# Performance work log

Measured on AMD Instinct MI355X. Metric: run time of the kernel, lower is better.

## Reference

```python
import jax, jax.numpy as jnp
import numpy as np

T = 512          # sentence length
D_IN = 449       # 300 (google w2v) + 100 (trained w2v) + 49 (len(cposTable))
H = 512          # lstm hidden_dim
H2 = 256         # hidden_dim2 (mlp head/modifier dim)


def _run_lstm(x, Wih, Whh, b):
    # single-direction LSTM, torch gate order (i, f, g, o); bias = b_ih + b_hh folded.
    hdim = Whh.shape[-1]
    def step(carry, xt):
        h, c = carry
        z = Wih @ xt + Whh @ h + b              # [4H]
        i, f, g, o = jnp.split(z, 4)
        c = jax.nn.sigmoid(f) * c + jax.nn.sigmoid(i) * jnp.tanh(g)
        h = jax.nn.sigmoid(o) * jnp.tanh(c)
        return (h, c), h
    h0 = jnp.zeros((hdim,), x.dtype)
    _, hs = jax.lax.scan(step, (h0, h0), x)
    return hs                                    # [T, H]


def _bilstm_layer(x, Wih, Whh, b):
    # Wih: [2, 4H, Din]; dir 0 forward, dir 1 backward
    fwd = _run_lstm(x, Wih[0], Whh[0], b[0])
    bwd = _run_lstm(x[::-1], Wih[1], Whh[1], b[1])[::-1]
    return jnp.concatenate([fwd, bwd], axis=-1)  # [T, 2H]


def setup_inputs() -> dict:
    key = jax.random.key(0)
    ks = jax.random.split(key, 20)
    s = 0.1  # keep LSTM gates out of deep saturation
    inp = {
        "x": jax.random.normal(ks[0], (T, D_IN), jnp.float32),
        "e1l0_Wih": s * jax.random.normal(ks[1], (2, 4 * H, D_IN), jnp.float32),
        "e1l0_Whh": s * jax.random.normal(ks[2], (2, 4 * H, H), jnp.float32),
        "e1l0_b":   s * jax.random.normal(ks[3], (2, 4 * H), jnp.float32),
        "e1l1_Wih": s * jax.random.normal(ks[4], (2, 4 * H, 2 * H), jnp.float32),
        "e1l1_Whh": s * jax.random.normal(ks[5], (2, 4 * H, H), jnp.float32),
        "e1l1_b":   s * jax.random.normal(ks[6], (2, 4 * H), jnp.float32),
        "e2l0_Wih": s * jax.random.normal(ks[7], (2, 4 * H, 2 * H), jnp.float32),
        "e2l0_Whh": s * jax.random.normal(ks[8], (2, 4 * H, H), jnp.float32),
        "e2l0_b":   s * jax.random.normal(ks[9], (2, 4 * H), jnp.float32),
        "e2l1_Wih": s * jax.random.normal(ks[10], (2, 4 * H, 2 * H), jnp.float32),
        "e2l1_Whh": s * jax.random.normal(ks[11], (2, 4 * H, H), jnp.float32),
        "e2l1_b":   s * jax.random.normal(ks[12], (2, 4 * H), jnp.float32),
        "Wh": s * jax.random.normal(ks[13], (H2, 2 * H), jnp.float32),
        "bh": s * jax.random.normal(ks[14], (H2,), jnp.float32),
        "Wm": s * jax.random.normal(ks[15], (H2, 2 * H), jnp.float32),
        "bm": s * jax.random.normal(ks[16], (H2,), jnp.float32),
        "w_score": s * jax.random.normal(ks[17], (H2,), jnp.float32),
        "b_score": s * jax.random.normal(ks[18], (1,), jnp.float32),
    }
    return inp


def reference(x, e1l0_Wih, e1l0_Whh, e1l0_b, e1l1_Wih, e1l1_Whh, e1l1_b,
              e2l0_Wih, e2l0_Whh, e2l0_b, e2l1_Wih, e2l1_Whh, e2l1_b,
              Wh, bh, Wm, bm, w_score, b_score):
    # encoder 1 (2-layer bi-LSTM); dropout is inference-mode identity
    h = _bilstm_layer(x, e1l0_Wih, e1l0_Whh, e1l0_b)
    h = _bilstm_layer(h, e1l1_Wih, e1l1_Whh, e1l1_b)
    # encoder 2 (2-layer bi-LSTM)
    h = _bilstm_layer(h, e2l0_Wih, e2l0_Whh, e2l0_b)
    h = _bilstm_layer(h, e2l1_Wih, e2l1_Whh, e2l1_b)
    # prepend zero ROOT row -> [T+1, 2H]
    h = jnp.concatenate([jnp.zeros((1, h.shape[1]), h.dtype), h], axis=0)
    # vectorized all-pairs edge scorer: tanh(heads[i] + mods[j]) @ w + b
    heads = h @ Wh.T + bh                         # [N, H2]
    mods = h @ Wm.T + bm                          # [N, H2]
    pair = jnp.tanh(heads[:, None, :] + mods[None, :, :])   # [N, N, H2]
    score = jnp.einsum('ijh,h->ij', pair, w_score) + b_score[0]
    n = score.shape[0]
    eye = jnp.eye(n, dtype=bool)
    score = jnp.where(eye, jnp.zeros((), score.dtype), score)  # diag = 0
    return score                                   # [T+1, T+1]
```

## Files before the change

kernel.cpp:

```cpp
#include <hip/hip_runtime.h>
#include <math.h>

#define TLEN 512
#define G4   2048
#define HID  512
#define D2H  1024
#define MLP  256
#define NR   513
#define NWG  32

typedef unsigned long long ull;

__device__ __forceinline__ float sigm(float x) { return 1.0f / (1.0f + __expf(-x)); }
__device__ __forceinline__ float tanh_(float x) { return 1.0f - 2.0f / (1.0f + __expf(2.0f * x)); }

__global__ __launch_bounds__(256) void pad_rows(const float* __restrict__ src,
                                                float* __restrict__ dst,
                                                int rows, int ksrc, int kdst) {
    int idx = blockIdx.x * 256 + threadIdx.x;
    if (idx >= rows * kdst) return;
    int r = idx / kdst, k = idx - r * kdst;
    dst[idx] = (k < ksrc) ? src[(long)r * ksrc + k] : 0.0f;
}

__global__ __launch_bounds__(256) void gemm_btn(
    const float* __restrict__ X, int ldx,
    const float* __restrict__ W, int ldw, long wsd,
    const float* __restrict__ bias, int bsd,
    float* __restrict__ Out, long osd,
    int M, int N, int K)
{
    int dir = blockIdx.z;
    const float* Wd = W + (long)dir * wsd;
    const float* bd = bias + (long)dir * bsd;
    float* Od = Out + (long)dir * osd;
    int n0 = blockIdx.x * 64, m0 = blockIdx.y * 64;
    __shared__ float As[16][68], Bs[16][68];
    int tid = threadIdx.x;
    int ti = tid >> 4, tj = tid & 15;
    int lr = tid >> 2, lq = tid & 3;
    float acc[4][4] = {};
    for (int k0 = 0; k0 < K; k0 += 16) {
        int mrow = m0 + lr;
        float4 xa = make_float4(0.f, 0.f, 0.f, 0.f);
        if (mrow < M) xa = *(const float4*)(X + (long)mrow * ldx + k0 + lq * 4);
        As[lq * 4 + 0][lr] = xa.x; As[lq * 4 + 1][lr] = xa.y;
        As[lq * 4 + 2][lr] = xa.z; As[lq * 4 + 3][lr] = xa.w;
        float4 wa = *(const float4*)(Wd + (long)(n0 + lr) * ldw + k0 + lq * 4);
        Bs[lq * 4 + 0][lr] = wa.x; Bs[lq * 4 + 1][lr] = wa.y;
        Bs[lq * 4 + 2][lr] = wa.z; Bs[lq * 4 + 3][lr] = wa.w;
        __syncthreads();
#pragma unroll
        for (int kk = 0; kk < 16; ++kk) {
            float4 a = *(const float4*)&As[kk][ti * 4];
            float4 b = *(const float4*)&Bs[kk][tj * 4];
            acc[0][0] += a.x * b.x; acc[0][1] += a.x * b.y; acc[0][2] += a.x * b.z; acc[0][3] += a.x * b.w;
            acc[1][0] += a.y * b.x; acc[1][1] += a.y * b.y; acc[1][2] += a.y * b.z; acc[1][3] += a.y * b.w;
            acc[2][0] += a.z * b.x; acc[2][1] += a.z * b.y; acc[2][2] += a.z * b.z; acc[2][3] += a.z * b.w;
            acc[3][0] += a.w * b.x; acc[3][1] += a.w * b.y; acc[3][2] += a.w * b.z; acc[3][3] += a.w * b.w;
        }
        __syncthreads();
    }
#pragma unroll
    for (int i = 0; i < 4; ++i) {
        int m = m0 + ti * 4 + i;
        if (m < M) {
#pragma unroll
            for (int j = 0; j < 4; ++j) {
                int n = n0 + tj * 4 + j;
                Od[(long)m * N + n] = acc[i][j] + bd[n];
            }
        }
    }
}

__global__ __launch_bounds__(256, 1) void lstm_rec(
    const float* __restrict__ Whh,
    const float* __restrict__ Zpre,
    ull* __restrict__ Ytag,
    float* __restrict__ Hout,
    unsigned tagbase)
{
    int wg = blockIdx.x;
    int dir = blockIdx.y;
    int tid = threadIdx.x;
    int rl = tid >> 2;
    int kp = tid & 3;
    int g = rl >> 4;
    int jj = rl & 15;
    int row_global = g * 512 + wg * 16 + jj;

    const float* wrow = Whh + ((long)dir * G4 + row_global) * HID + kp * 128;
    float4 w4[32];
#pragma unroll
    for (int u = 0; u < 32; ++u) w4[u] = *(const float4*)(wrow + u * 4);

    __shared__ float hs[528];
    __shared__ float zs[64];
    float c_reg = 0.0f;

    for (int s = 0; s < TLEN; ++s) {
        int t_x = dir ? (TLEN - 1 - s) : s;
        float z_i = 0.f, z_f = 0.f, z_g = 0.f, z_o = 0.f;
        if (tid < 16) {
            const float* zp = Zpre + ((long)dir * TLEN + t_x) * G4 + wg * 16 + tid;
            z_i = zp[0]; z_f = zp[512]; z_g = zp[1024]; z_o = zp[1536];
        }
        if (s > 0) {
            int rrow = dir ? (TLEN - s) : (s - 1);
            const ull* src = Ytag + (long)rrow * D2H + dir * HID;
            unsigned expect = tagbase + (unsigned)rrow;
            int e = tid * 2;
            ull v0 = __hip_atomic_load(src + e, __ATOMIC_RELAXED, __HIP_MEMORY_SCOPE_AGENT);
            while ((unsigned)(v0 >> 32) != expect) {
                __builtin_amdgcn_s_sleep(1);
                v0 = __hip_atomic_load(src + e, __ATOMIC_RELAXED, __HIP_MEMORY_SCOPE_AGENT);
            }
            ull v1 = __hip_atomic_load(src + e + 1, __ATOMIC_RELAXED, __HIP_MEMORY_SCOPE_AGENT);
            while ((unsigned)(v1 >> 32) != expect) {
                __builtin_amdgcn_s_sleep(1);
                v1 = __hip_atomic_load(src + e + 1, __ATOMIC_RELAXED, __HIP_MEMORY_SCOPE_AGENT);
            }
            int base = e + (e >> 7) * 4;
            hs[base]     = __uint_as_float((unsigned)v0);
            hs[base + 1] = __uint_as_float((unsigned)v1);
            __syncthreads();
            const float* hp = &hs[kp * 132];
            float z = 0.0f;
#pragma unroll
            for (int u = 0; u < 32; ++u) {
                float4 hv = *(const float4*)(hp + u * 4);
                z = fmaf(w4[u].x, hv.x, z); z = fmaf(w4[u].y, hv.y, z);
                z = fmaf(w4[u].z, hv.z, z); z = fmaf(w4[u].w, hv.w, z);
            }
            z += __shfl_xor(z, 1);
            z += __shfl_xor(z, 2);
            if (kp == 0) zs[rl] = z;
            __syncthreads();
        } else {
            if (tid < 64) zs[tid] = 0.0f;
            __syncthreads();
        }
        if (tid < 16) {
            float zi = zs[tid]      + z_i;
            float zf = zs[16 + tid] + z_f;
            float zg = zs[32 + tid] + z_g;
            float zo = zs[48 + tid] + z_o;
            float ig = sigm(zi), fg = sigm(zf), gv = tanh_(zg), og = sigm(zo);
            c_reg = fg * c_reg + ig * gv;
            float h = og * tanh_(c_reg);
            int j = wg * 16 + tid;
            ull pk = ((ull)(tagbase + (unsigned)t_x) << 32) | (ull)__float_as_uint(h);
            __hip_atomic_store(Ytag + (long)t_x * D2H + dir * HID + j, pk,
                               __ATOMIC_RELAXED, __HIP_MEMORY_SCOPE_AGENT);
            Hout[(long)t_x * D2H + dir * HID + j] = h;
        }
    }
}

__global__ __launch_bounds__(256) void pair_score(
    const float* __restrict__ heads, const float* __restrict__ mods,
    const float* __restrict__ w_s, const float* __restrict__ b_s,
    float* __restrict__ out)
{
    __shared__ float hsh[16][260], msh[16][260], wsh[256];
    int tid = threadIdx.x;
    int i0 = blockIdx.y * 16, j0 = blockIdx.x * 16;
    int r = tid >> 4, cq = tid & 15;
#pragma unroll
    for (int u = 0; u < 4; ++u) {
        int col = cq * 16 + u * 4;
        if (col < MLP) {
            float4 hv = make_float4(0.f, 0.f, 0.f, 0.f), mv = hv;
            if (i0 + r < NR) hv = *(const float4*)(heads + (long)(i0 + r) * MLP + col);
            if (j0 + r < NR) mv = *(const float4*)(mods + (long)(j0 + r) * MLP + col);
            *(float4*)&hsh[r][col] = hv;
            *(float4*)&msh[r][col] = mv;
        }
    }
    wsh[tid] = w_s[tid];
    __syncthreads();
    int ti = tid >> 4, tj = tid & 15;
    float acc = 0.0f;
#pragma unroll 4
    for (int h = 0; h < MLP; ++h) {
        acc += wsh[h] * tanh_(hsh[ti][h] + msh[tj][h]);
    }
    int i = i0 + ti, j = j0 + tj;
    if (i < NR && j < NR) out[(long)i * NR + j] = (i == j) ? 0.0f : (acc + b_s[0]);
}

extern "C" void kernel_launch(void* const* d_in, const int* in_sizes, int n_in,
                              void* d_out, int out_size, void* d_ws, size_t ws_size,
                              hipStream_t stream)
{
    const float* x = (const float*)d_in[0];
    float* ws = (float*)d_ws;
    float* Xpad  = ws;
    float* Wpad  = Xpad + 512 * 512;
    float* Z     = Wpad + 2 * 2048 * 512;
    ull*   YtagA = (ull*)(Z + 2 * 512 * 2048);
    ull*   YtagB = YtagA + 512 * 1024;
    float* bufAc = (float*)(YtagB + 512 * 1024);
    float* bufBc = bufAc + 512 * 1024;
    float* Hcat  = bufBc + 512 * 1024;
    float* heads = Hcat + 513 * 1024;
    float* mods  = heads + 513 * 256;

    hipMemsetAsync(YtagA, 0, 2 * 512 * 1024 * sizeof(ull), stream);
    hipMemsetAsync(Hcat, 0, D2H * sizeof(float), stream);

    pad_rows<<<dim3(1024), 256, 0, stream>>>(x, Xpad, 512, 449, 512);
    pad_rows<<<dim3(8192), 256, 0, stream>>>((const float*)d_in[1], Wpad, 2 * 2048, 449, 512);

    dim3 gz(G4 / 64, TLEN / 64, 2);
    dim3 gr(NWG, 2);

    gemm_btn<<<gz, 256, 0, stream>>>(Xpad, 512, Wpad, 512, (long)G4 * 512,
                                     (const float*)d_in[3], G4, Z, (long)TLEN * G4, TLEN, G4, 512);
    lstm_rec<<<gr, 256, 0, stream>>>((const float*)d_in[2], Z, YtagA, bufAc, 1u * 4096u);

    gemm_btn<<<gz, 256, 0, stream>>>(bufAc, D2H, (const float*)d_in[4], D2H, (long)G4 * D2H,
                                     (const float*)d_in[6], G4, Z, (long)TLEN * G4, TLEN, G4, D2H);
    lstm_rec<<<gr, 256, 0, stream>>>((const float*)d_in[5], Z, YtagB, bufBc, 2u * 4096u);

    gemm_btn<<<gz, 256, 0, stream>>>(bufBc, D2H, (const float*)d_in[7], D2H, (long)G4 * D2H,
                                     (const float*)d_in[9], G4, Z, (long)TLEN * G4, TLEN, G4, D2H);
    lstm_rec<<<gr, 256, 0, stream>>>((const float*)d_in[8], Z, YtagA, bufAc, 3u * 4096u);

    gemm_btn<<<gz, 256, 0, stream>>>(bufAc, D2H, (const float*)d_in[10], D2H, (long)G4 * D2H,
                                     (const float*)d_in[12], G4, Z, (long)TLEN * G4, TLEN, G4, D2H);
    lstm_rec<<<gr, 256, 0, stream>>>((const float*)d_in[11], Z, YtagB, Hcat + D2H, 4u * 4096u);

    gemm_btn<<<dim3(MLP / 64, 9, 1), 256, 0, stream>>>(Hcat, D2H, (const float*)d_in[13], D2H, 0,
                                                       (const float*)d_in[14], 0, heads, 0, NR, MLP, D2H);
    gemm_btn<<<dim3(MLP / 64, 9, 1), 256, 0, stream>>>(Hcat, D2H, (const float*)d_in[15], D2H, 0,
                                                       (const float*)d_in[16], 0, mods, 0, NR, MLP, D2H);

    pair_score<<<dim3(33, 33), 256, 0, stream>>>(heads, mods, (const float*)d_in[17],
                                                 (const float*)d_in[18], (float*)d_out);
}
```

Before: 4.477 ms.

## Spread LSTM recurrence over 128 workgroups per direction, reading Whh from cache

The recurrent kernel now uses 128 workgroups per direction instead of 32, each owning 4 hidden units (16 gate rows). Each gate row is split across 16 threads that reduce with shuffles. The Whh weights are no longer held in registers and are reloaded from global memory (L2/cache) every step. The intent is to shorten per-step latency and use more CUs, at the cost of more cross-workgroup polling on the tagged h vector and repeated weight reads each step. It assumes all 256 workgroups stay co-resident.

```diff
diff --git a/kernel.cpp b/kernel.cpp
--- a/kernel.cpp
+++ b/kernel.cpp
@@ -7,7 +7,7 @@
 #define D2H  1024
 #define MLP  256
 #define NR   513
-#define NWG  32
+#define NWG  128
 
 typedef unsigned long long ull;
 
@@ -84,26 +84,22 @@
     int wg = blockIdx.x;
     int dir = blockIdx.y;
     int tid = threadIdx.x;
-    int rl = tid >> 2;
-    int kp = tid & 3;
-    int g = rl >> 4;
-    int jj = rl & 15;
-    int row_global = g * 512 + wg * 16 + jj;
-
-    const float* wrow = Whh + ((long)dir * G4 + row_global) * HID + kp * 128;
-    float4 w4[32];
-#pragma unroll
-    for (int u = 0; u < 32; ++u) w4[u] = *(const float4*)(wrow + u * 4);
-
-    __shared__ float hs[528];
-    __shared__ float zs[64];
+    int c = tid & 15;
+    int r = tid >> 4;
+    int g = r >> 2, i = r & 3;
+    int rowg = g * 512 + wg * 4 + i;
+
+    const float* pw = Whh + ((long)dir * G4 + rowg) * HID + c * 32;
+
+    __shared__ float hs[576];
+    __shared__ float zs[16];
     float c_reg = 0.0f;
 
     for (int s = 0; s < TLEN; ++s) {
         int t_x = dir ? (TLEN - 1 - s) : s;
         float z_i = 0.f, z_f = 0.f, z_g = 0.f, z_o = 0.f;
-        if (tid < 16) {
-            const float* zp = Zpre + ((long)dir * TLEN + t_x) * G4 + wg * 16 + tid;
+        if (tid < 4) {
+            const float* zp = Zpre + ((long)dir * TLEN + t_x) * G4 + wg * 4 + tid;
             z_i = zp[0]; z_f = zp[512]; z_g = zp[1024]; z_o = zp[1536];
         }
         if (s > 0) {
@@ -111,45 +107,51 @@
             const ull* src = Ytag + (long)rrow * D2H + dir * HID;
             unsigned expect = tagbase + (unsigned)rrow;
             int e = tid * 2;
-            ull v0 = __hip_atomic_load(src + e, __ATOMIC_RELAXED, __HIP_MEMORY_SCOPE_AGENT);
+            ull v0 = __hip_atomic_load(src + e,     __ATOMIC_RELAXED, __HIP_MEMORY_SCOPE_AGENT);
+            ull v1 = __hip_atomic_load(src + e + 1, __ATOMIC_RELAXED, __HIP_MEMORY_SCOPE_AGENT);
             while ((unsigned)(v0 >> 32) != expect) {
                 __builtin_amdgcn_s_sleep(1);
                 v0 = __hip_atomic_load(src + e, __ATOMIC_RELAXED, __HIP_MEMORY_SCOPE_AGENT);
             }
-            ull v1 = __hip_atomic_load(src + e + 1, __ATOMIC_RELAXED, __HIP_MEMORY_SCOPE_AGENT);
             while ((unsigned)(v1 >> 32) != expect) {
                 __builtin_amdgcn_s_sleep(1);
                 v1 = __hip_atomic_load(src + e + 1, __ATOMIC_RELAXED, __HIP_MEMORY_SCOPE_AGENT);
             }
-            int base = e + (e >> 7) * 4;
+            int base = e + ((e >> 5) << 2);
             hs[base]     = __uint_as_float((unsigned)v0);
             hs[base + 1] = __uint_as_float((unsigned)v1);
             __syncthreads();
-            const float* hp = &hs[kp * 132];
-            float z = 0.0f;
-#pragma unroll
-            for (int u = 0; u < 32; ++u) {
-                float4 hv = *(const float4*)(hp + u * 4);
-                z = fmaf(w4[u].x, hv.x, z); z = fmaf(w4[u].y, hv.y, z);
-                z = fmaf(w4[u].z, hv.z, z); z = fmaf(w4[u].w, hv.w, z);
-            }
-            z += __shfl_xor(z, 1);
-            z += __shfl_xor(z, 2);
-            if (kp == 0) zs[rl] = z;
+            const float* hp = &hs[c * 36];
+            float a0 = 0.f, a1 = 0.f;
+#pragma unroll
+            for (int u = 0; u < 8; u += 2) {
+                float4 w0 = *(const float4*)(pw + u * 4);
+                float4 h0 = *(const float4*)(hp + u * 4);
+                float4 w1 = *(const float4*)(pw + u * 4 + 4);
+                float4 h1 = *(const float4*)(hp + u * 4 + 4);
+                a0 = fmaf(w0.x, h0.x, a0); a0 = fmaf(w0.y, h0.y, a0);
+                a0 = fmaf(w0.z, h0.z, a0); a0 = fmaf(w0.w, h0.w, a0);
+                a1 = fmaf(w1.x, h1.x, a1); a1 = fmaf(w1.y, h1.y, a1);
+                a1 = fmaf(w1.z, h1.z, a1); a1 = fmaf(w1.w, h1.w, a1);
+            }
+            float z = a0 + a1;
+            z += __shfl_xor(z, 1); z += __shfl_xor(z, 2);
+            z += __shfl_xor(z, 4); z += __shfl_xor(z, 8);
+            if (c == 0) zs[r] = z;
             __syncthreads();
         } else {
-            if (tid < 64) zs[tid] = 0.0f;
+            if (tid < 16) zs[tid] = 0.0f;
             __syncthreads();
         }
-        if (tid < 16) {
+        if (tid < 4) {
             float zi = zs[tid]      + z_i;
-            float zf = zs[16 + tid] + z_f;
-            float zg = zs[32 + tid] + z_g;
-            float zo = zs[48 + tid] + z_o;
+            float zf = zs[4 + tid]  + z_f;
+            float zg = zs[8 + tid]  + z_g;
+            float zo = zs[12 + tid] + z_o;
             float ig = sigm(zi), fg = sigm(zf), gv = tanh_(zg), og = sigm(zo);
             c_reg = fg * c_reg + ig * gv;
             float h = og * tanh_(c_reg);
-            int j = wg * 16 + tid;
+            int j = wg * 4 + tid;
             ull pk = ((ull)(tagbase + (unsigned)t_x) << 32) | (ull)__float_as_uint(h);
             __hip_atomic_store(Ytag + (long)t_x * D2H + dir * HID + j, pk,
                                __ATOMIC_RELAXED, __HIP_MEMORY_SCOPE_AGENT);
```

New measurement: 6.546 ms. +46.2%, slower.
